# Kernel tuning notes

Hardware: AMD Instinct MI355X
Metric: run time of the kernel (lower is better)

Reference implementation:

```python
import jax, jax.numpy as jnp
import numpy as np
import math

N, E, IN, C, H, ED, B = 50000, 800000, 64, 32, 4, 1, 64
HC = H * C
EPS = 1e-5


def setup_inputs() -> dict:
    key = jax.random.key(0)
    ks = jax.random.split(key, 16)
    def lin(k, fan_in, fan_out):
        s = 1.0 / math.sqrt(fan_in)
        return jax.random.normal(k, (fan_in, fan_out), jnp.float32) * s
    inp = {
        "x": jax.random.normal(ks[0], (N, IN), jnp.float32),
        "edge_index": jax.random.randint(ks[1], (2, E), 0, N, jnp.int64),
        "edge_attr": jax.random.normal(ks[2], (E, ED), jnp.float32),
        "batch_index": jnp.sort(jax.random.randint(ks[3], (N,), 0, B, jnp.int64)),
        # TransformerConv params
        "Wq": lin(ks[4], IN, HC), "bq": jnp.zeros((HC,), jnp.float32),
        "Wk": lin(ks[5], IN, HC), "bk": jnp.zeros((HC,), jnp.float32),
        "Wv": lin(ks[6], IN, HC), "bv": jnp.zeros((HC,), jnp.float32),
        "We": lin(ks[7], ED, HC), "be": jnp.zeros((HC,), jnp.float32),
        "Wskip": lin(ks[8], IN, HC), "bskip": jnp.zeros((HC,), jnp.float32),
        "Wbeta": lin(ks[9], 3 * HC, 1),
        # post linear: H*C -> C
        "Wlin": lin(ks[10], HC, C), "blin": jnp.zeros((C,), jnp.float32),
        # GraphNorm params
        "gn_weight": jnp.ones((C,), jnp.float32),
        "gn_bias": jnp.zeros((C,), jnp.float32),
        "gn_mean_scale": jnp.ones((C,), jnp.float32),
    }
    return inp


def reference(x, edge_index, edge_attr, batch_index, Wq, bq, Wk, bk, Wv, bv,
              We, be, Wskip, bskip, Wbeta, Wlin, blin,
              gn_weight, gn_bias, gn_mean_scale):
    src, dst = edge_index[0], edge_index[1]
    # dense projections [N, H, C]
    q = (x @ Wq + bq).reshape(N, H, C)
    k = (x @ Wk + bk).reshape(N, H, C)
    v = (x @ Wv + bv).reshape(N, H, C)
    e = (edge_attr @ We + be).reshape(E, H, C)
    # per-edge attention logits [E, H]
    k_e = k[src] + e
    alpha = jnp.einsum('ehc,ehc->eh', q[dst], k_e) / math.sqrt(C)
    # segment softmax over incoming edges of each dst node
    m = jax.ops.segment_max(alpha, dst, num_segments=N)  # [N, H]
    a = jnp.exp(alpha - m[dst])
    denom = jax.ops.segment_sum(a, dst, num_segments=N)  # [N, H]
    a = a / jnp.maximum(denom, 1e-16)[dst]
    # (dropout p=0.3 on attention is a no-op in eval mode)
    msg = (v[src] + e) * a[:, :, None]                    # [E, H, C]
    out = jax.ops.segment_sum(msg, dst, num_segments=N).reshape(N, HC)
    # beta-gated skip connection
    x_r = x @ Wskip + bskip                               # [N, HC]
    beta = jax.nn.sigmoid(jnp.concatenate([out, x_r, out - x_r], -1) @ Wbeta)
    out = beta * x_r + (1.0 - beta) * out
    # linear + relu
    h = jax.nn.relu(out @ Wlin + blin)                    # [N, C]
    # GraphNorm over per-graph segments
    ones = jnp.ones((N, 1), h.dtype)
    cnt = jax.ops.segment_sum(ones, batch_index, num_segments=B)  # [B, 1]
    cnt = jnp.maximum(cnt, 1.0)
    mean = jax.ops.segment_sum(h, batch_index, num_segments=B) / cnt
    centered = h - mean[batch_index] * gn_mean_scale
    var = jax.ops.segment_sum(centered * centered, batch_index, num_segments=B) / cnt
    std = jnp.sqrt(var + EPS)
    return gn_weight * centered / std[batch_index] + gn_bias
```

## Files before the change

kernel.cpp:

```cpp
#include <hip/hip_runtime.h>
#include <math.h>

static constexpr int kN  = 50000;
static constexpr int kE  = 800000;
static constexpr int kC  = 32;
static constexpr int kH  = 4;
static constexpr int kHC = 128;
static constexpr int kB  = 64;
static constexpr int kNB = (kN + 255) / 256;
static constexpr int kMB = (kN + 127) / 128;

typedef __attribute__((ext_vector_type(8))) short bf16x8;
typedef __attribute__((ext_vector_type(4))) float f32x4;

__device__ __forceinline__ unsigned short f2bf(float f) {
    unsigned u = __float_as_uint(f);
    unsigned r = (u + 0x7FFFu + ((u >> 16) & 1u)) >> 16;
    return (unsigned short)r;
}
__device__ __forceinline__ float blo(unsigned u) { return __uint_as_float(u << 16); }
__device__ __forceinline__ float bhi(unsigned u) { return __uint_as_float(u & 0xFFFF0000u); }

__global__ __launch_bounds__(256) void proj_mfma_kernel(
    const float4* __restrict__ x4,
    const float* __restrict__ Wq, const float* __restrict__ bq,
    const float* __restrict__ Wk, const float* __restrict__ bk,
    const float* __restrict__ Wv, const float* __restrict__ bv,
    const float* __restrict__ Wskip, const float* __restrict__ bskip,
    unsigned short* __restrict__ qxb, unsigned short* __restrict__ kvb)
{
    __shared__ uint4 lds[128 * 8 + 512 * 8];
    uint4* xsS = lds;
    uint4* wtS = lds + 128 * 8;
    const int t = threadIdx.x;
    const int w = t >> 6;
    const int l = t & 63;
    const int l15 = l & 15, l16 = l >> 4;
    const int n0 = blockIdx.x * 128;

    {
        uint2* xs2 = (uint2*)xsS;
#pragma unroll
        for (int i = 0; i < 8; ++i) {
            int fi = i * 256 + t;
            int row = fi >> 4, f4 = fi & 15;
            int n = n0 + row;
            float4 v = make_float4(0.f, 0.f, 0.f, 0.f);
            if (n < kN) v = x4[(size_t)n * 16 + f4];
            unsigned u0 = f2bf(v.x) | ((unsigned)f2bf(v.y) << 16);
            unsigned u1 = f2bf(v.z) | ((unsigned)f2bf(v.w) << 16);
            int slot = (row * 8 + (f4 >> 1)) ^ (row & 7);
            xs2[slot * 2 + (f4 & 1)] = make_uint2(u0, u1);
        }
    }
    {
        unsigned short* wtU = (unsigned short*)wtS;
#pragma unroll
        for (int it = 0; it < 32; ++it) {
            int flat = it * 256 + t;
            int m = flat >> 11, rem = flat & 2047;
            int k = rem >> 5, j4 = rem & 31;
            const float* Wm = (m == 0) ? Wq : (m == 1) ? Wk : (m == 2) ? Wv : Wskip;
            float4 v = *(const float4*)&Wm[k * kHC + j4 * 4];
#pragma unroll
            for (int jj = 0; jj < 4; ++jj) {
                int col = m * 128 + j4 * 4 + jj;
                float f = (jj == 0) ? v.x : (jj == 1) ? v.y : (jj == 2) ? v.z : v.w;
                int slot = (col * 8 + (k >> 3)) ^ (col & 7);
                wtU[slot * 8 + (k & 7)] = f2bf(f);
            }
        }
    }
    __syncthreads();

    const float* Bm = (w == 0) ? bq : (w == 1) ? bk : (w == 2) ? bv : bskip;
    float bias[8];
#pragma unroll
    for (int c = 0; c < 8; ++c) bias[c] = Bm[c * 16 + l15];

    unsigned short* dst = (w == 0 || w == 3) ? qxb : kvb;
    const int add4 = (w >= 2) ? 4 : 0;

    for (int rt = 0; rt < 4; ++rt) {
        f32x4 acc[2][8];
#pragma unroll
        for (int r = 0; r < 2; ++r)
#pragma unroll
            for (int c = 0; c < 8; ++c)
                acc[r][c] = (f32x4){bias[c], bias[c], bias[c], bias[c]};
#pragma unroll
        for (int kk = 0; kk < 2; ++kk) {
            int row0 = rt * 32 + l15;
            int row1 = row0 + 16;
            uint4 a0u = xsS[(row0 * 8 + kk * 4 + l16) ^ (row0 & 7)];
            uint4 a1u = xsS[(row1 * 8 + kk * 4 + l16) ^ (row1 & 7)];
            bf16x8 a0 = __builtin_bit_cast(bf16x8, a0u);
            bf16x8 a1 = __builtin_bit_cast(bf16x8, a1u);
#pragma unroll
            for (int c = 0; c < 8; ++c) {
                int col = w * 128 + c * 16 + l15;
                uint4 bu = wtS[(col * 8 + kk * 4 + l16) ^ (col & 7)];
                bf16x8 b = __builtin_bit_cast(bf16x8, bu);
                acc[0][c] = __builtin_amdgcn_mfma_f32_16x16x32_bf16(a0, b, acc[0][c], 0, 0, 0);
                acc[1][c] = __builtin_amdgcn_mfma_f32_16x16x32_bf16(a1, b, acc[1][c], 0, 0, 0);
            }
        }
#pragma unroll
        for (int r = 0; r < 2; ++r) {
#pragma unroll
            for (int j = 0; j < 4; ++j) {
                int node = n0 + rt * 32 + r * 16 + l16 * 4 + j;
                bool valid = (node < kN) && ((l & 1) == 0);
                size_t base = (size_t)node * 128;
#pragma unroll
                for (int c = 0; c < 8; ++c) {
                    float v0 = acc[r][c][j];
                    float v1 = __shfl_xor(v0, 1);
                    if (valid) {
                        int jcol = c * 16 + l15;
                        int gpos = ((jcol >> 2) << 3) | (jcol & 3);
                        unsigned pk = f2bf(v0) | ((unsigned)f2bf(v1) << 16);
                        ((unsigned*)dst)[base + ((gpos + add4) >> 1)] = pk;
                    }
                }
            }
        }
    }
}

__global__ __launch_bounds__(256) void hist_kernel(
    const int* __restrict__ ei, int* __restrict__ deg)
{
    int i = blockIdx.x * 256 + threadIdx.x;
    if (i < kE) atomicAdd(&deg[ei[kE + i]], 1);
}

__global__ __launch_bounds__(256) void scanA_kernel(
    const int* __restrict__ deg, int* __restrict__ bsum)
{
    int i = blockIdx.x * 256 + threadIdx.x;
    int v = (i < kN) ? deg[i] : 0;
#pragma unroll
    for (int s = 1; s < 64; s <<= 1) v += __shfl_xor(v, s);
    __shared__ int sh[4];
    if ((threadIdx.x & 63) == 0) sh[threadIdx.x >> 6] = v;
    __syncthreads();
    if (threadIdx.x == 0) bsum[blockIdx.x] = sh[0] + sh[1] + sh[2] + sh[3];
}

__global__ __launch_bounds__(256) void scanB_kernel(
    const int* __restrict__ bsum, int* __restrict__ bofs, int* __restrict__ rowptr)
{
    __shared__ int sh[256];
    int t = threadIdx.x;
    int v = (t < kNB) ? bsum[t] : 0;
    sh[t] = v; __syncthreads();
    for (int off = 1; off < 256; off <<= 1) {
        int u = (t >= off) ? sh[t - off] : 0;
        __syncthreads();
        sh[t] += u;
        __syncthreads();
    }
    if (t < kNB) bofs[t] = sh[t] - v;
    if (t == kNB - 1) rowptr[kN] = sh[t];
}

__global__ __launch_bounds__(256) void scanC_kernel(
    const int* __restrict__ deg, const int* __restrict__ bofs,
    int* __restrict__ rowptr, int* __restrict__ cursor)
{
    __shared__ int sh[256];
    int t = threadIdx.x, i = blockIdx.x * 256 + t;
    int v = (i < kN) ? deg[i] : 0;
    sh[t] = v; __syncthreads();
    for (int off = 1; off < 256; off <<= 1) {
        int u = (t >= off) ? sh[t - off] : 0;
        __syncthreads();
        sh[t] += u;
        __syncthreads();
    }
    if (i < kN) {
        int ex = sh[t] - v + bofs[blockIdx.x];
        rowptr[i] = ex;
        cursor[i] = ex;
    }
}

__global__ __launch_bounds__(256) void scatter_kernel(
    const int* __restrict__ ei, const float* __restrict__ ea,
    int* __restrict__ cursor, int2* __restrict__ csr)
{
    int i = blockIdx.x * 256 + threadIdx.x;
    if (i >= kE) return;
    int dst = ei[kE + i];
    int slot = atomicAdd(&cursor[dst], 1);
    csr[slot] = make_int2(ei[i], __float_as_int(ea[i]));
}

__global__ __launch_bounds__(256) void node_attn_kernel(
    const int* __restrict__ rowptr, const int2* __restrict__ csr,
    const unsigned short* __restrict__ qxb, const unsigned short* __restrict__ kvb,
    const float* __restrict__ We, const float* __restrict__ be,
    const float* __restrict__ Wbeta, const float* __restrict__ Wlin,
    const float* __restrict__ blin, float* __restrict__ hbuf)
{
    __shared__ float wlS[kHC * kC];
    __shared__ float wbS[3 * kHC];
    __shared__ float oshS[4][kHC];
    const int t = threadIdx.x, wv = t >> 6, lane = t & 63;
    for (int i = t; i < kHC * kC; i += 256) wlS[i] = Wlin[i];
    for (int i = t; i < 3 * kHC; i += 256) wbS[i] = Wbeta[i];
    __syncthreads();

    const int node = blockIdx.x * 4 + wv;
    const int half = lane >> 5;
    const int sl   = lane & 31;
    const int ch   = sl * 4;
    const float4 we4 = *(const float4*)&We[ch];
    const float4 be4 = *(const float4*)&be[ch];
    const float4 wbA = *(const float4*)&wbS[ch];
    const float4 wbB = *(const float4*)&wbS[kHC + ch];
    const float4 wbC = *(const float4*)&wbS[2 * kHC + ch];
    const float blc = blin[sl];
    const float A = 0.17677669529663687f;

    const uint4 qx = *((const uint4*)(qxb + (size_t)node * 256) + sl);
    const float q0 = blo(qx.x), q1 = bhi(qx.x), q2v = blo(qx.y), q3 = bhi(qx.y);
    const float xr0 = blo(qx.z), xr1 = bhi(qx.z), xr2 = blo(qx.w), xr3 = bhi(qx.w);
    float qw = q0 * we4.x + q1 * we4.y + q2v * we4.z + q3 * we4.w;
    float qe = q0 * be4.x + q1 * be4.y + q2v * be4.z + q3 * be4.w;
    qw += __shfl_xor(qw, 1); qe += __shfl_xor(qe, 1);
    qw += __shfl_xor(qw, 2); qe += __shfl_xor(qe, 2);
    qw += __shfl_xor(qw, 4); qe += __shfl_xor(qe, 4);
    const float qwA = qw * A, qbA = qe * A;

    float mx = -3.0e38f, ss = 0.f, swa = 0.f;
    float ax0 = 0.f, ax1 = 0.f, ax2 = 0.f, ax3 = 0.f;
    const int beg = rowptr[node], end = rowptr[node + 1];
    int e = beg;
    for (; e + 7 < end; e += 8) {
        int2 cA = csr[e + half];
        int2 cB = csr[e + 2 + half];
        int2 cC = csr[e + 4 + half];
        int2 cD = csr[e + 6 + half];
        const uint4 uA = *((const uint4*)(kvb + (size_t)cA.x * 256) + sl);
        const uint4 uB = *((const uint4*)(kvb + (size_t)cB.x * 256) + sl);
        const uint4 uC = *((const uint4*)(kvb + (size_t)cC.x * 256) + sl);
        const uint4 uD = *((const uint4*)(kvb + (size_t)cD.x * 256) + sl);
        float aA = __int_as_float(cA.y), aB = __int_as_float(cB.y);
        float aC = __int_as_float(cC.y), aD = __int_as_float(cD.y);
        float pA = fmaf(q3, bhi(uA.y), fmaf(q2v, blo(uA.y), fmaf(q1, bhi(uA.x), q0 * blo(uA.x))));
        float pB = fmaf(q3, bhi(uB.y), fmaf(q2v, blo(uB.y), fmaf(q1, bhi(uB.x), q0 * blo(uB.x))));
        float pC = fmaf(q3, bhi(uC.y), fmaf(q2v, blo(uC.y), fmaf(q1, bhi(uC.x), q0 * blo(uC.x))));
        float pD = fmaf(q3, bhi(uD.y), fmaf(q2v, blo(uD.y), fmaf(q1, bhi(uD.x), q0 * blo(uD.x))));
        pA += __shfl_xor(pA, 1); pB += __shfl_xor(pB, 1); pC += __shfl_xor(pC, 1); pD += __shfl_xor(pD, 1);
        pA += __shfl_xor(pA, 2); pB += __shfl_xor(pB, 2); pC += __shfl_xor(pC, 2); pD += __shfl_xor(pD, 2);
        pA += __shfl_xor(pA, 4); pB += __shfl_xor(pB, 4); pC += __shfl_xor(pC, 4); pD += __shfl_xor(pD, 4);
        float lA = fmaf(pA, A, fmaf(aA, qwA, qbA));
        float lB = fmaf(pB, A, fmaf(aB, qwA, qbA));
        float lC = fmaf(pC, A, fmaf(aC, qwA, qbA));
        float lD = fmaf(pD, A, fmaf(aD, qwA, qbA));
        float bm = fmaxf(fmaxf(fmaxf(lA, lB), fmaxf(lC, lD)), mx);
        float sc = __expf(mx - bm);
        float eA = __expf(lA - bm), eB = __expf(lB - bm);
        float eC = __expf(lC - bm), eD = __expf(lD - bm);
        ss  = fmaf(ss , sc, (eA + eB) + (eC + eD));
        swa = fmaf(swa, sc, fmaf(eA, aA, fmaf(eB, aB, fmaf(eC, aC, eD * aD))));
        ax0 = fmaf(ax0, sc, fmaf(eA, blo(uA.z), fmaf(eB, blo(uB.z), fmaf(eC, blo(uC.z), eD * blo(uD.z)))));
        ax1 = fmaf(ax1, sc, fmaf(eA, bhi(uA.z), fmaf(eB, bhi(uB.z), fmaf(eC, bhi(uC.z), eD * bhi(uD.z)))));
        ax2 = fmaf(ax2, sc, fmaf(eA, blo(uA.w), fmaf(eB, blo(uB.w), fmaf(eC, blo(uC.w), eD * blo(uD.w)))));
        ax3 = fmaf(ax3, sc, fmaf(eA, bhi(uA.w), fmaf(eB, bhi(uB.w), fmaf(eC, bhi(uC.w), eD * bhi(uD.w)))));
        mx = bm;
    }
    for (; e < end; e += 2) {
        int idx = e + half;
        bool valid = idx < end;
        int2 cA = csr[valid ? idx : end - 1];
        const uint4 uA = *((const uint4*)(kvb + (size_t)cA.x * 256) + sl);
        float aA = __int_as_float(cA.y);
        float pA = fmaf(q3, bhi(uA.y), fmaf(q2v, blo(uA.y), fmaf(q1, bhi(uA.x), q0 * blo(uA.x))));
        pA += __shfl_xor(pA, 1);
        pA += __shfl_xor(pA, 2);
        pA += __shfl_xor(pA, 4);
        float lA = valid ? fmaf(pA, A, fmaf(aA, qwA, qbA)) : -3.0e38f;
        float bm = fmaxf(lA, mx);
        float sc = __expf(mx - bm);
        float eA = valid ? __expf(lA - bm) : 0.f;
        ss  = fmaf(ss , sc, eA);
        swa = fmaf(swa, sc, eA * aA);
        ax0 = fmaf(ax0, sc, eA * blo(uA.z));
        ax1 = fmaf(ax1, sc, eA * bhi(uA.z));
        ax2 = fmaf(ax2, sc, eA * blo(uA.w));
        ax3 = fmaf(ax3, sc, eA * bhi(uA.w));
        mx = bm;
    }
    {
        float mo = __shfl_xor(mx, 32);
        float bm = fmaxf(mx, mo);
        float sc = __expf(mx - bm);
        ss *= sc; swa *= sc; ax0 *= sc; ax1 *= sc; ax2 *= sc; ax3 *= sc;
        ss  += __shfl_xor(ss , 32);
        swa += __shfl_xor(swa, 32);
        ax0 += __shfl_xor(ax0, 32);
        ax1 += __shfl_xor(ax1, 32);
        ax2 += __shfl_xor(ax2, 32);
        ax3 += __shfl_xor(ax3, 32);
    }
    float rcp = 1.f / fmaxf(ss, 1e-16f);
    float v0 = fmaf(swa, we4.x, fmaf(ss, be4.x, ax0)) * rcp;
    float v1 = fmaf(swa, we4.y, fmaf(ss, be4.y, ax1)) * rcp;
    float v2 = fmaf(swa, we4.z, fmaf(ss, be4.z, ax2)) * rcp;
    float v3 = fmaf(swa, we4.w, fmaf(ss, be4.w, ax3)) * rcp;
    float part = wbA.x * v0 + wbA.y * v1 + wbA.z * v2 + wbA.w * v3
               + wbB.x * xr0 + wbB.y * xr1 + wbB.z * xr2 + wbB.w * xr3
               + wbC.x * (v0 - xr0) + wbC.y * (v1 - xr1)
               + wbC.z * (v2 - xr2) + wbC.w * (v3 - xr3);
    part += __shfl_xor(part, 1);
    part += __shfl_xor(part, 2);
    part += __shfl_xor(part, 4);
    part += __shfl_xor(part, 8);
    part += __shfl_xor(part, 16);
    float beta = 1.f / (1.f + __expf(-part));
    float o0 = beta * xr0 + (1.f - beta) * v0;
    float o1 = beta * xr1 + (1.f - beta) * v1;
    float o2 = beta * xr2 + (1.f - beta) * v2;
    float o3 = beta * xr3 + (1.f - beta) * v3;
    if (half == 0) *(float4*)&oshS[wv][ch] = make_float4(o0, o1, o2, o3);
    __builtin_amdgcn_wave_barrier();
    float hp = 0.f;
#pragma unroll
    for (int jj = 0; jj < 64; ++jj) {
        int j = half * 64 + jj;
        hp = fmaf(oshS[wv][j], wlS[j * kC + sl], hp);
    }
    hp += __shfl_xor(hp, 32);
    if (lane < 32) hbuf[(size_t)node * kC + sl] = fmaxf(hp + blc, 0.f);
}

__global__ __launch_bounds__(256) void gn_reduce_kernel(
    const float* __restrict__ hbuf, const int* __restrict__ batch,
    const float* __restrict__ gms, float* __restrict__ stats)
{
    const int g = blockIdx.x;
    const int t = threadIdx.x;
    __shared__ int se[2];
    __shared__ float s1[8][kC], s2[8][kC];
    if (t < 2) {
        int target = g + t;
        int lo = 0, hi = kN;
        while (lo < hi) { int mid = (lo + hi) >> 1; if (batch[mid] < target) lo = mid + 1; else hi = mid; }
        se[t] = lo;
    }
    __syncthreads();
    int start = se[0], end = se[1];
    float cnt = fmaxf((float)(end - start), 1.f);
    int c = t & 31, r = t >> 5;
    float a = 0.f, b = 0.f;
    for (int n = start + r; n < end; n += 8) {
        float v = hbuf[(size_t)n * kC + c];
        a += v; b = fmaf(v, v, b);
    }
    s1[r][c] = a; s2[r][c] = b;
    __syncthreads();
    if (t < kC) {
        float sa = 0.f, sb = 0.f;
#pragma unroll
        for (int i = 0; i < 8; ++i) { sa += s1[i][t]; sb += s2[i][t]; }
        float mean = sa / cnt;
        float ms   = mean * gms[t];
        float var  = sb / cnt - 2.f * ms * mean + ms * ms;
        stats[g * 64 + t]      = ms;
        stats[g * 64 + 32 + t] = rsqrtf(var + 1e-5f);
    }
}

__global__ __launch_bounds__(256) void gn_apply_kernel(
    const float* __restrict__ hbuf, const int* __restrict__ batch,
    const float* __restrict__ stats,
    const float* __restrict__ gw, const float* __restrict__ gb,
    float* __restrict__ out)
{
    int idx = blockIdx.x * 256 + threadIdx.x;
    if (idx >= kN * kC) return;
    int n = idx >> 5, c = idx & 31;
    int g = batch[n];
    float ms   = stats[g * 64 + c];
    float rstd = stats[g * 64 + 32 + c];
    float v = hbuf[idx];
    out[idx] = fmaf(gw[c] * (v - ms), rstd, gb[c]);
}

extern "C" void kernel_launch(void* const* d_in, const int* in_sizes, int n_in,
                              void* d_out, int out_size, void* d_ws, size_t ws_size,
                              hipStream_t stream) {
    (void)in_sizes; (void)n_in; (void)out_size; (void)ws_size;
    const float* x     = (const float*)d_in[0];
    const int*   ei    = (const int*)d_in[1];
    const float* ea    = (const float*)d_in[2];
    const int*   batch = (const int*)d_in[3];
    const float* Wq    = (const float*)d_in[4];
    const float* bq    = (const float*)d_in[5];
    const float* Wk    = (const float*)d_in[6];
    const float* bk    = (const float*)d_in[7];
    const float* Wv    = (const float*)d_in[8];
    const float* bv    = (const float*)d_in[9];
    const float* We    = (const float*)d_in[10];
    const float* be    = (const float*)d_in[11];
    const float* Wskip = (const float*)d_in[12];
    const float* bskip = (const float*)d_in[13];
    const float* Wbeta = (const float*)d_in[14];
    const float* Wlin  = (const float*)d_in[15];
    const float* blin  = (const float*)d_in[16];
    const float* gw    = (const float*)d_in[17];
    const float* gb    = (const float*)d_in[18];
    const float* gms   = (const float*)d_in[19];
    float* out = (float*)d_out;

    char* ws = (char*)d_ws;
    int2*  csr    = (int2*)ws;            ws += (size_t)kE * 8;
    unsigned short* qxb = (unsigned short*)ws; ws += (size_t)kN * 256 * 2;
    unsigned short* kvb = (unsigned short*)ws; ws += (size_t)kN * 256 * 2;
    float* hbuf   = (float*)ws;           ws += (size_t)kN * kC * 4;
    int*   deg    = (int*)ws;             ws += (size_t)kN * 4;
    int*   cursor = (int*)ws;             ws += (size_t)kN * 4;
    int*   rowptr = (int*)ws;             ws += (size_t)(kN + 1) * 4;
    int*   bsum   = (int*)ws;             ws += (size_t)kNB * 4;
    int*   bofs   = (int*)ws;             ws += (size_t)kNB * 4;
    float* stats  = (float*)ws;           ws += (size_t)kB * 64 * 4;

    hipMemsetAsync(deg, 0, (size_t)kN * 4, stream);

    hist_kernel<<<(kE + 255) / 256, 256, 0, stream>>>(ei, deg);
    proj_mfma_kernel<<<kMB, 256, 0, stream>>>(
        (const float4*)x, Wq, bq, Wk, bk, Wv, bv, Wskip, bskip, qxb, kvb);
    scanA_kernel<<<kNB, 256, 0, stream>>>(deg, bsum);
    scanB_kernel<<<1, 256, 0, stream>>>(bsum, bofs, rowptr);
    scanC_kernel<<<kNB, 256, 0, stream>>>(deg, bofs, rowptr, cursor);
    scatter_kernel<<<(kE + 255) / 256, 256, 0, stream>>>(ei, ea, cursor, csr);
    node_attn_kernel<<<kN / 4, 256, 0, stream>>>(
        rowptr, csr, qxb, kvb, We, be, Wbeta, Wlin, blin, hbuf);
    gn_reduce_kernel<<<kB, 256, 0, stream>>>(hbuf, batch, gms, stats);
    gn_apply_kernel<<<(kN * kC + 255) / 256, 256, 0, stream>>>(
        hbuf, batch, stats, gw, gb, out);
}
```

Baseline: 260.7 us.

## Fuse hist/weight-pack, projection/scanA and scan kernels; unroll edge loop by four

Weight packing into MFMA fragment order moves into the histogram launch. The projection now keeps B fragments in registers and reads x straight from global memory, with no LDS staging. The scanA work is appended as extra blocks of the projection launch. scanB is merged into scanC, where every block redoes the small block-sum scan. Together these cut launches and per-block weight conversion. The attention edge loop unroll drops from 8 to 4, which lowers register pressure but gives less memory-level parallelism per iteration.

```diff
diff --git a/kernel.cpp b/kernel.cpp
--- a/kernel.cpp
+++ b/kernel.cpp
@@ -21,57 +21,65 @@
 __device__ __forceinline__ float blo(unsigned u) { return __uint_as_float(u << 16); }
 __device__ __forceinline__ float bhi(unsigned u) { return __uint_as_float(u & 0xFFFF0000u); }
 
-__global__ __launch_bounds__(256) void proj_mfma_kernel(
+__global__ __launch_bounds__(256) void hist_packw_kernel(
+    const int* __restrict__ ei, int* __restrict__ deg,
+    const float* __restrict__ Wq, const float* __restrict__ Wk,
+    const float* __restrict__ Wv, const float* __restrict__ Wskip,
+    uint4* __restrict__ wtf)
+{
+    if (blockIdx.x < 16) {
+        int tid = blockIdx.x * 256 + threadIdx.x;
+        int f = tid >> 6, l = tid & 63;
+        int m = f >> 4, c = (f >> 1) & 7, kk = f & 1;
+        int col = c * 16 + (l & 15);
+        int k0  = kk * 32 + (l >> 4) * 8;
+        const float* Wm = (m == 0) ? Wq : (m == 1) ? Wk : (m == 2) ? Wv : Wskip;
+        unsigned p[4];
+#pragma unroll
+        for (int j = 0; j < 4; ++j) {
+            unsigned lo = f2bf(Wm[(k0 + 2 * j) * kHC + col]);
+            unsigned hi = f2bf(Wm[(k0 + 2 * j + 1) * kHC + col]);
+            p[j] = lo | (hi << 16);
+        }
+        wtf[f * 64 + l] = make_uint4(p[0], p[1], p[2], p[3]);
+        return;
+    }
+    int i = (blockIdx.x - 16) * 256 + threadIdx.x;
+    if (i < kE) atomicAdd(&deg[ei[kE + i]], 1);
+}
+
+__global__ __launch_bounds__(256) void proj_scanA_kernel(
     const float4* __restrict__ x4,
-    const float* __restrict__ Wq, const float* __restrict__ bq,
-    const float* __restrict__ Wk, const float* __restrict__ bk,
-    const float* __restrict__ Wv, const float* __restrict__ bv,
-    const float* __restrict__ Wskip, const float* __restrict__ bskip,
-    unsigned short* __restrict__ qxb, unsigned short* __restrict__ kvb)
-{
-    __shared__ uint4 lds[128 * 8 + 512 * 8];
-    uint4* xsS = lds;
-    uint4* wtS = lds + 128 * 8;
+    const float* __restrict__ bq, const float* __restrict__ bk,
+    const float* __restrict__ bv, const float* __restrict__ bskip,
+    const uint4* __restrict__ wtf,
+    unsigned short* __restrict__ qxb, unsigned short* __restrict__ kvb,
+    const int* __restrict__ deg, int* __restrict__ bsum)
+{
+    __shared__ int sh4[4];
+    if (blockIdx.x >= kMB) {
+        int bid = blockIdx.x - kMB;
+        int i = bid * 256 + threadIdx.x;
+        int v = (i < kN) ? deg[i] : 0;
+#pragma unroll
+        for (int s = 1; s < 64; s <<= 1) v += __shfl_xor(v, s);
+        if ((threadIdx.x & 63) == 0) sh4[threadIdx.x >> 6] = v;
+        __syncthreads();
+        if (threadIdx.x == 0) bsum[bid] = sh4[0] + sh4[1] + sh4[2] + sh4[3];
+        return;
+    }
     const int t = threadIdx.x;
     const int w = t >> 6;
     const int l = t & 63;
     const int l15 = l & 15, l16 = l >> 4;
     const int n0 = blockIdx.x * 128;
 
-    {
-        uint2* xs2 = (uint2*)xsS;
-#pragma unroll
-        for (int i = 0; i < 8; ++i) {
-            int fi = i * 256 + t;
-            int row = fi >> 4, f4 = fi & 15;
-            int n = n0 + row;
-            float4 v = make_float4(0.f, 0.f, 0.f, 0.f);
-            if (n < kN) v = x4[(size_t)n * 16 + f4];
-            unsigned u0 = f2bf(v.x) | ((unsigned)f2bf(v.y) << 16);
-            unsigned u1 = f2bf(v.z) | ((unsigned)f2bf(v.w) << 16);
-            int slot = (row * 8 + (f4 >> 1)) ^ (row & 7);
-            xs2[slot * 2 + (f4 & 1)] = make_uint2(u0, u1);
-        }
-    }
-    {
-        unsigned short* wtU = (unsigned short*)wtS;
-#pragma unroll
-        for (int it = 0; it < 32; ++it) {
-            int flat = it * 256 + t;
-            int m = flat >> 11, rem = flat & 2047;
-            int k = rem >> 5, j4 = rem & 31;
-            const float* Wm = (m == 0) ? Wq : (m == 1) ? Wk : (m == 2) ? Wv : Wskip;
-            float4 v = *(const float4*)&Wm[k * kHC + j4 * 4];
-#pragma unroll
-            for (int jj = 0; jj < 4; ++jj) {
-                int col = m * 128 + j4 * 4 + jj;
-                float f = (jj == 0) ? v.x : (jj == 1) ? v.y : (jj == 2) ? v.z : v.w;
-                int slot = (col * 8 + (k >> 3)) ^ (col & 7);
-                wtU[slot * 8 + (k & 7)] = f2bf(f);
-            }
-        }
-    }
-    __syncthreads();
+    bf16x8 bf[8][2];
+#pragma unroll
+    for (int c = 0; c < 8; ++c)
+#pragma unroll
+        for (int kk = 0; kk < 2; ++kk)
+            bf[c][kk] = __builtin_bit_cast(bf16x8, wtf[(unsigned)((w * 16 + c * 2 + kk) * 64 + l)]);
 
     const float* Bm = (w == 0) ? bq : (w == 1) ? bk : (w == 2) ? bv : bskip;
     float bias[8];
@@ -82,6 +90,8 @@
     const int add4 = (w >= 2) ? 4 : 0;
 
     for (int rt = 0; rt < 4; ++rt) {
+        const int r0 = n0 + rt * 32 + l15;
+        const int r1 = r0 + 16;
         f32x4 acc[2][8];
 #pragma unroll
         for (int r = 0; r < 2; ++r)
@@ -90,19 +100,31 @@
                 acc[r][c] = (f32x4){bias[c], bias[c], bias[c], bias[c]};
 #pragma unroll
         for (int kk = 0; kk < 2; ++kk) {
-            int row0 = rt * 32 + l15;
-            int row1 = row0 + 16;
-            uint4 a0u = xsS[(row0 * 8 + kk * 4 + l16) ^ (row0 & 7)];
-            uint4 a1u = xsS[(row1 * 8 + kk * 4 + l16) ^ (row1 & 7)];
-            bf16x8 a0 = __builtin_bit_cast(bf16x8, a0u);
-            bf16x8 a1 = __builtin_bit_cast(bf16x8, a1u);
+            float4 xa0 = make_float4(0.f,0.f,0.f,0.f), xb0 = xa0, xa1 = xa0, xb1 = xa0;
+            if (r0 < kN) {
+                xa0 = x4[(size_t)r0 * 16 + kk * 8 + l16 * 2];
+                xb0 = x4[(size_t)r0 * 16 + kk * 8 + l16 * 2 + 1];
+            }
+            if (r1 < kN) {
+                xa1 = x4[(size_t)r1 * 16 + kk * 8 + l16 * 2];
+                xb1 = x4[(size_t)r1 * 16 + kk * 8 + l16 * 2 + 1];
+            }
+            uint4 u0 = make_uint4(
+                f2bf(xa0.x) | ((unsigned)f2bf(xa0.y) << 16),
+                f2bf(xa0.z) | ((unsigned)f2bf(xa0.w) << 16),
+                f2bf(xb0.x) | ((unsigned)f2bf(xb0.y) << 16),
+                f2bf(xb0.z) | ((unsigned)f2bf(xb0.w) << 16));
+            uint4 u1 = make_uint4(
+                f2bf(xa1.x) | ((unsigned)f2bf(xa1.y) << 16),
+                f2bf(xa1.z) | ((unsigned)f2bf(xa1.w) << 16),
+                f2bf(xb1.x) | ((unsigned)f2bf(xb1.y) << 16),
+                f2bf(xb1.z) | ((unsigned)f2bf(xb1.w) << 16));
+            bf16x8 a0 = __builtin_bit_cast(bf16x8, u0);
+            bf16x8 a1 = __builtin_bit_cast(bf16x8, u1);
 #pragma unroll
             for (int c = 0; c < 8; ++c) {
-                int col = w * 128 + c * 16 + l15;
-                uint4 bu = wtS[(col * 8 + kk * 4 + l16) ^ (col & 7)];
-                bf16x8 b = __builtin_bit_cast(bf16x8, bu);
-                acc[0][c] = __builtin_amdgcn_mfma_f32_16x16x32_bf16(a0, b, acc[0][c], 0, 0, 0);
-                acc[1][c] = __builtin_amdgcn_mfma_f32_16x16x32_bf16(a1, b, acc[1][c], 0, 0, 0);
+                acc[0][c] = __builtin_amdgcn_mfma_f32_16x16x32_bf16(a0, bf[c][kk], acc[0][c], 0, 0, 0);
+                acc[1][c] = __builtin_amdgcn_mfma_f32_16x16x32_bf16(a1, bf[c][kk], acc[1][c], 0, 0, 0);
             }
         }
 #pragma unroll
@@ -128,49 +150,23 @@
     }
 }
 
-__global__ __launch_bounds__(256) void hist_kernel(
-    const int* __restrict__ ei, int* __restrict__ deg)
-{
-    int i = blockIdx.x * 256 + threadIdx.x;
-    if (i < kE) atomicAdd(&deg[ei[kE + i]], 1);
-}
-
-__global__ __launch_bounds__(256) void scanA_kernel(
-    const int* __restrict__ deg, int* __restrict__ bsum)
-{
-    int i = blockIdx.x * 256 + threadIdx.x;
-    int v = (i < kN) ? deg[i] : 0;
-#pragma unroll
-    for (int s = 1; s < 64; s <<= 1) v += __shfl_xor(v, s);
-    __shared__ int sh[4];
-    if ((threadIdx.x & 63) == 0) sh[threadIdx.x >> 6] = v;
-    __syncthreads();
-    if (threadIdx.x == 0) bsum[blockIdx.x] = sh[0] + sh[1] + sh[2] + sh[3];
-}
-
-__global__ __launch_bounds__(256) void scanB_kernel(
-    const int* __restrict__ bsum, int* __restrict__ bofs, int* __restrict__ rowptr)
-{
+__global__ __launch_bounds__(256) void scanC2_kernel(
+    const int* __restrict__ deg, const int* __restrict__ bsum,
+    int* __restrict__ rowptr, int* __restrict__ cursor)
+{
+    __shared__ int bsh[256];
     __shared__ int sh[256];
-    int t = threadIdx.x;
-    int v = (t < kNB) ? bsum[t] : 0;
-    sh[t] = v; __syncthreads();
+    const int t = threadIdx.x, i = blockIdx.x * 256 + t;
+    int bv = (t < kNB) ? bsum[t] : 0;
+    bsh[t] = bv; __syncthreads();
     for (int off = 1; off < 256; off <<= 1) {
-        int u = (t >= off) ? sh[t - off] : 0;
+        int u = (t >= off) ? bsh[t - off] : 0;
         __syncthreads();
-        sh[t] += u;
+        bsh[t] += u;
         __syncthreads();
     }
-    if (t < kNB) bofs[t] = sh[t] - v;
-    if (t == kNB - 1) rowptr[kN] = sh[t];
-}
-
-__global__ __launch_bounds__(256) void scanC_kernel(
-    const int* __restrict__ deg, const int* __restrict__ bofs,
-    int* __restrict__ rowptr, int* __restrict__ cursor)
-{
-    __shared__ int sh[256];
-    int t = threadIdx.x, i = blockIdx.x * 256 + t;
+    const int bofs = (blockIdx.x == 0) ? 0 : bsh[blockIdx.x - 1];
+    if (blockIdx.x == 0 && t == 0) rowptr[kN] = bsh[kNB - 1];
     int v = (i < kN) ? deg[i] : 0;
     sh[t] = v; __syncthreads();
     for (int off = 1; off < 256; off <<= 1) {
@@ -180,7 +176,7 @@
         __syncthreads();
     }
     if (i < kN) {
-        int ex = sh[t] - v + bofs[blockIdx.x];
+        int ex = sh[t] - v + bofs;
         rowptr[i] = ex;
         cursor[i] = ex;
     }
@@ -238,38 +234,28 @@
     float ax0 = 0.f, ax1 = 0.f, ax2 = 0.f, ax3 = 0.f;
     const int beg = rowptr[node], end = rowptr[node + 1];
     int e = beg;
-    for (; e + 7 < end; e += 8) {
+    for (; e + 3 < end; e += 4) {
         int2 cA = csr[e + half];
         int2 cB = csr[e + 2 + half];
-        int2 cC = csr[e + 4 + half];
-        int2 cD = csr[e + 6 + half];
         const uint4 uA = *((const uint4*)(kvb + (size_t)cA.x * 256) + sl);
         const uint4 uB = *((const uint4*)(kvb + (size_t)cB.x * 256) + sl);
-        const uint4 uC = *((const uint4*)(kvb + (size_t)cC.x * 256) + sl);
-        const uint4 uD = *((const uint4*)(kvb + (size_t)cD.x * 256) + sl);
         float aA = __int_as_float(cA.y), aB = __int_as_float(cB.y);
-        float aC = __int_as_float(cC.y), aD = __int_as_float(cD.y);
         float pA = fmaf(q3, bhi(uA.y), fmaf(q2v, blo(uA.y), fmaf(q1, bhi(uA.x), q0 * blo(uA.x))));
         float pB = fmaf(q3, bhi(uB.y), fmaf(q2v, blo(uB.y), fmaf(q1, bhi(uB.x), q0 * blo(uB.x))));
-        float pC = fmaf(q3, bhi(uC.y), fmaf(q2v, blo(uC.y), fmaf(q1, bhi(uC.x), q0 * blo(uC.x))));
-        float pD = fmaf(q3, bhi(uD.y), fmaf(q2v, blo(uD.y), fmaf(q1, bhi(uD.x), q0 * blo(uD.x))));
-        pA += __shfl_xor(pA, 1); pB += __shfl_xor(pB, 1); pC += __shfl_xor(pC, 1); pD += __shfl_xor(pD, 1);
-        pA += __shfl_xor(pA, 2); pB += __shfl_xor(pB, 2); pC += __shfl_xor(pC, 2); pD += __shfl_xor(pD, 2);
-        pA += __shfl_xor(pA, 4); pB += __shfl_xor(pB, 4); pC += __shfl_xor(pC, 4); pD += __shfl_xor(pD, 4);
+        pA += __shfl_xor(pA, 1); pB += __shfl_xor(pB, 1);
+        pA += __shfl_xor(pA, 2); pB += __shfl_xor(pB, 2);
+        pA += __shfl_xor(pA, 4); pB += __shfl_xor(pB, 4);
         float lA = fmaf(pA, A, fmaf(aA, qwA, qbA));
         float lB = fmaf(pB, A, fmaf(aB, qwA, qbA));
-        float lC = fmaf(pC, A, fmaf(aC, qwA, qbA));
-        float lD = fmaf(pD, A, fmaf(aD, qwA, qbA));
-        float bm = fmaxf(fmaxf(fmaxf(lA, lB), fmaxf(lC, lD)), mx);
+        float bm = fmaxf(fmaxf(lA, lB), mx);
         float sc = __expf(mx - bm);
         float eA = __expf(lA - bm), eB = __expf(lB - bm);
-        float eC = __expf(lC - bm), eD = __expf(lD - bm);
-        ss  = fmaf(ss , sc, (eA + eB) + (eC + eD));
-        swa = fmaf(swa, sc, fmaf(eA, aA, fmaf(eB, aB, fmaf(eC, aC, eD * aD))));
-        ax0 = fmaf(ax0, sc, fmaf(eA, blo(uA.z), fmaf(eB, blo(uB.z), fmaf(eC, blo(uC.z), eD * blo(uD.z)))));
-        ax1 = fmaf(ax1, sc, fmaf(eA, bhi(uA.z), fmaf(eB, bhi(uB.z), fmaf(eC, bhi(uC.z), eD * bhi(uD.z)))));
-        ax2 = fmaf(ax2, sc, fmaf(eA, blo(uA.w), fmaf(eB, blo(uB.w), fmaf(eC, blo(uC.w), eD * blo(uD.w)))));
-        ax3 = fmaf(ax3, sc, fmaf(eA, bhi(uA.w), fmaf(eB, bhi(uB.w), fmaf(eC, bhi(uC.w), eD * bhi(uD.w)))));
+        ss  = fmaf(ss , sc, eA + eB);
+        swa = fmaf(swa, sc, fmaf(eA, aA, eB * aB));
+        ax0 = fmaf(ax0, sc, fmaf(eA, blo(uA.z), eB * blo(uB.z)));
+        ax1 = fmaf(ax1, sc, fmaf(eA, bhi(uA.z), eB * bhi(uB.z)));
+        ax2 = fmaf(ax2, sc, fmaf(eA, blo(uA.w), eB * blo(uB.w)));
+        ax3 = fmaf(ax3, sc, fmaf(eA, bhi(uA.w), eB * bhi(uB.w)));
         mx = bm;
     }
     for (; e < end; e += 2) {
@@ -425,17 +411,16 @@
     int*   cursor = (int*)ws;             ws += (size_t)kN * 4;
     int*   rowptr = (int*)ws;             ws += (size_t)(kN + 1) * 4;
     int*   bsum   = (int*)ws;             ws += (size_t)kNB * 4;
-    int*   bofs   = (int*)ws;             ws += (size_t)kNB * 4;
     float* stats  = (float*)ws;           ws += (size_t)kB * 64 * 4;
+    uint4* wtf    = (uint4*)ws;           ws += (size_t)64 * 64 * 16;
 
     hipMemsetAsync(deg, 0, (size_t)kN * 4, stream);
 
-    hist_kernel<<<(kE + 255) / 256, 256, 0, stream>>>(ei, deg);
-    proj_mfma_kernel<<<kMB, 256, 0, stream>>>(
-        (const float4*)x, Wq, bq, Wk, bk, Wv, bv, Wskip, bskip, qxb, kvb);
-    scanA_kernel<<<kNB, 256, 0, stream>>>(deg, bsum);
-    scanB_kernel<<<1, 256, 0, stream>>>(bsum, bofs, rowptr);
-    scanC_kernel<<<kNB, 256, 0, stream>>>(deg, bofs, rowptr, cursor);
+    hist_packw_kernel<<<16 + (kE + 255) / 256, 256, 0, stream>>>(
+        ei, deg, Wq, Wk, Wv, Wskip, wtf);
+    proj_scanA_kernel<<<kMB + kNB, 256, 0, stream>>>(
+        (const float4*)x, bq, bk, bv, bskip, wtf, qxb, kvb, deg, bsum);
+    scanC2_kernel<<<kNB, 256, 0, stream>>>(deg, bsum, rowptr, cursor);
     scatter_kernel<<<(kE + 255) / 256, 256, 0, stream>>>(ei, ea, cursor, csr);
     node_attn_kernel<<<kN / 4, 256, 0, stream>>>(
         rowptr, csr, qxb, kvb, We, be, Wbeta, Wlin, blin, hbuf);
```

Measured after the change: 236.6 us. 9.2% less time.
